# Kernel optimization log

Hardware: AMD Instinct MI355X
Metric: run time of the kernel (lower is better)

Reference implementation:

```python
import jax, jax.numpy as jnp
import numpy as np

B, C, H, W = 8, 512, 64, 64
RED = 4
CR = C // RED  # 128

def setup_inputs() -> dict:
    key = jax.random.key(0)
    k1, k2, k3 = jax.random.split(key, 3)
    x = jax.random.normal(k1, (B, C, H, W), dtype=jnp.float32)
    # conv_in: 1x1 conv, no bias -> weight [3*CR, C]
    w_in = jax.random.normal(k2, (3 * CR, C), dtype=jnp.float32) * 0.02
    # conv_out: 1x1 conv, no bias -> weight [C, CR]
    w_out = jax.random.normal(k3, (C, CR), dtype=jnp.float32) * 0.02
    return {"x": x, "w_in": w_in, "w_out": w_out}

def reference(x, w_in, w_out):
    b, c, h, w = x.shape
    n = h * w
    xf = x.reshape(b, c, n)                         # flatten spatial -> [B,C,N]
    proj = jnp.einsum('oc,bcn->bon', w_in, xf)      # 1x1 conv_in -> [B,3*CR,N]
    emb_a, emb_b, g = jnp.split(proj, 3, axis=1)    # each [B,CR,N]
    # unscaled full self-attention over N spatial tokens
    weights = jnp.einsum('bcn,bcm->bnm', emb_a, emb_b)   # [B,N,N]
    weights = jax.nn.softmax(weights, axis=2)
    y = jnp.einsum('bnm,bcm->bnc', weights, g)           # [B,N,CR]
    y = jnp.einsum('oc,bnc->bon', w_out, y)              # 1x1 conv_out -> [B,C,N]
    return x + y.reshape(b, c, h, w)
```

## Files before the change

### kernel.cpp

```cpp
#include <hip/hip_runtime.h>


typedef __attribute__((ext_vector_type(8))) short short8;
typedef __attribute__((ext_vector_type(4))) float f32x4;
typedef __attribute__((ext_vector_type(16))) float f32x16;
typedef __attribute__((ext_vector_type(2))) unsigned int uint2v;

__device__ inline unsigned bfr(float f) {
  union { float f; unsigned u; } v; v.f = f;
  return v.u + 0x8000u;
}
__device__ inline unsigned short f2bf(float f) { return (unsigned short)(bfr(f) >> 16); }
__device__ inline unsigned pack2(float a, float b) {
  return __builtin_amdgcn_perm(bfr(b), bfr(a), 0x07060302u);
}
__device__ inline unsigned cvtpk(float a, float b) {
  unsigned r;
  asm("v_cvt_pk_bf16_f32 %0, %1, %2" : "=v"(r) : "v"(a), "v"(b));
  return r;
}
__device__ inline int sw(int row, int col, int stride_halves) {
  return row * stride_halves + ((((col >> 3) ^ (row & 7)) << 3) | (col & 7));
}
__device__ inline void load_lds16(const void* g, void* l) {
  __builtin_amdgcn_global_load_lds(
      (const __attribute__((address_space(1))) unsigned int*)g,
      (__attribute__((address_space(3))) unsigned int*)l, 16, 0, 0);
}

__global__ __launch_bounds__(256) void k_prep(const float* __restrict__ w_in,
                                              const float* __restrict__ w_out,
                                              unsigned short* __restrict__ wi,
                                              unsigned short* __restrict__ wo) {
  int i = blockIdx.x * 256 + threadIdx.x;
  const float* src;
  unsigned short* dst;
  int base;
  float s = 1.0f;
  if (i < 24576) {
    src = w_in;  dst = wi; base = i * 8;
    if (base < 128 * 512) s = 1.4426950408889634f;
  } else {
    src = w_out; dst = wo; base = (i - 24576) * 8;
  }
  float4 d0 = *(const float4*)&src[base];
  float4 d1 = *(const float4*)&src[base + 4];
  d0.x *= s; d0.y *= s; d0.z *= s; d0.w *= s;
  d1.x *= s; d1.y *= s; d1.z *= s; d1.w *= s;
  uint4 p;
  p.x = pack2(d0.x, d0.y); p.y = pack2(d0.z, d0.w);
  p.z = pack2(d1.x, d1.y); p.w = pack2(d1.z, d1.w);
  *(uint4*)&dst[base] = p;
}

__global__ __launch_bounds__(256, 2) void k_proj(const float* __restrict__ x,
                                                 const unsigned short* __restrict__ wi,
                                                 unsigned short* __restrict__ aq,
                                                 unsigned short* __restrict__ Kf,
                                                 unsigned short* __restrict__ Vf) {
  __shared__ unsigned short A_lds[384 * 64];
  __shared__ unsigned short B_lds[64 * 64];
  const int t = threadIdx.x;
  const int lane = t & 63;
  const int w = t >> 6;
  const int l15 = lane & 15;
  const int quad = lane >> 4;
  const int tl = blockIdx.x;
  const int n0 = tl * 64;
  const int b = blockIdx.y;
  const int ch8g = t >> 5;
  const int tp = t & 31;

  f32x4 acc[6][4];
#pragma unroll
  for (int i = 0; i < 6; i++)
#pragma unroll
    for (int j = 0; j < 4; j++) acc[i][j] = (f32x4)0.f;

  float2 d[8];
#pragma unroll
  for (int j = 0; j < 8; j++)
    d[j] = *(const float2*)&x[((size_t)(b * 512 + ch8g * 8 + j)) * 4096 + n0 + tp * 2];

  for (int k0 = 0; k0 < 512; k0 += 64) {
#pragma unroll
    for (int j = 0; j < 12; j++) {
      int row = w * 96 + j * 8 + (lane >> 3);
      int gs = (lane & 7) ^ (row & 7);
      load_lds16(&wi[(size_t)row * 512 + k0 + gs * 8],
                 (void*)&A_lds[(w * 96 + j * 8) * 64]);
    }
#pragma unroll
    for (int i = 0; i < 2; i++) {
      int r = tp * 2 + i;
      uint4 pv;
      if (i == 0) {
        pv.x = pack2(d[0].x, d[1].x); pv.y = pack2(d[2].x, d[3].x);
        pv.z = pack2(d[4].x, d[5].x); pv.w = pack2(d[6].x, d[7].x);
      } else {
        pv.x = pack2(d[0].y, d[1].y); pv.y = pack2(d[2].y, d[3].y);
        pv.z = pack2(d[4].y, d[5].y); pv.w = pack2(d[6].y, d[7].y);
      }
      *(uint4*)&B_lds[sw(r, ch8g * 8, 64)] = pv;
    }
    if (k0 + 64 < 512) {
#pragma unroll
      for (int j = 0; j < 8; j++)
        d[j] = *(const float2*)&x[((size_t)(b * 512 + k0 + 64 + ch8g * 8 + j)) * 4096 + n0 + tp * 2];
    }
    __syncthreads();
#pragma unroll
    for (int kk = 0; kk < 64; kk += 32) {
      short8 a[6];
#pragma unroll
      for (int m = 0; m < 6; m++)
        a[m] = *(const short8*)&A_lds[sw(w * 96 + m * 16 + l15, kk + quad * 8, 64)];
#pragma unroll
      for (int ns = 0; ns < 4; ns++) {
        short8 bb = *(const short8*)&B_lds[sw(ns * 16 + l15, kk + quad * 8, 64)];
#pragma unroll
        for (int m = 0; m < 6; m++)
          acc[m][ns] = __builtin_amdgcn_mfma_f32_16x16x32_bf16(a[m], bb, acc[m][ns], 0, 0, 0);
      }
    }
    __syncthreads();
  }
  const size_t tbase = ((size_t)(b * 64 + tl)) * 8192;
#pragma unroll
  for (int m = 0; m < 6; m++) {
    int o = w * 96 + m * 16 + quad * 4;
    if (o < 128) {
#pragma unroll
      for (int ns = 0; ns < 4; ns++) {
        int n = n0 + ns * 16 + l15;
        uint2 p;
        p.x = pack2(acc[m][ns][0], acc[m][ns][1]);
        p.y = pack2(acc[m][ns][2], acc[m][ns][3]);
        *(uint2*)&aq[((size_t)(b * 4096 + n)) * 128 + o] = p;
      }
    } else if (o < 256) {
      int c = o - 128;
      int ksc = c >> 4, hk = (c >> 3) & 1, e0 = c & 7;
#pragma unroll
      for (int ns = 0; ns < 4; ns++) {
        int key = ns * 16 + l15;
        int ck = (key >> 5) * 8 + ksc;
        int lane_k = hk * 32 + (key & 31);
        uint2 p;
        p.x = pack2(acc[m][ns][0], acc[m][ns][1]);
        p.y = pack2(acc[m][ns][2], acc[m][ns][3]);
        *(uint2*)&Kf[tbase + ck * 512 + lane_k * 8 + e0] = p;
      }
    } else {
      int cb = o - 256;
#pragma unroll
      for (int ns = 0; ns < 4; ns++) {
        int key = ns * 16 + l15;
        int g8 = key >> 3;
        int e = key & 7;
        size_t kb = tbase + (size_t)((g8 & 1) * 32) * 8 + e + (size_t)(g8 >> 1) * 512;
#pragma unroll
        for (int r = 0; r < 4; r++) {
          int c = cb + r;
          Vf[kb + (size_t)(c >> 5) * 4 * 512 + (size_t)(c & 31) * 8] = f2bf(acc[m][ns][r]);
        }
      }
    }
  }
}

__global__ __launch_bounds__(512, 2) void k_attn(const unsigned short* __restrict__ aq,
                                                 const unsigned short* __restrict__ Kf,
                                                 const unsigned short* __restrict__ Vf,
                                                 unsigned short* __restrict__ yt) {
  __shared__ uint4 smem4[65536 / 16];
  unsigned short* smem_h = (unsigned short*)smem4;
  float* Obuf = (float*)smem4;
  float* lsumbuf = (float*)((char*)smem4 + 33024);
  unsigned* Pbuf = (unsigned*)((char*)smem4 + 33280);

  const int t = threadIdx.x;
  const int lane = t & 63;
  const int w = t >> 6;
  const int wr = w & 1;
  const int wc = w >> 1;
  const int l31 = lane & 31;
  const int h = lane >> 5;
  const int b = blockIdx.x & 7;
  const int q0 = (blockIdx.x >> 3) * 128;

  short8 qf[8];
  {
    const unsigned short* qp = &aq[((size_t)(b * 4096 + q0 + wc * 32 + l31)) * 128 + h * 8];
#pragma unroll
    for (int ks = 0; ks < 8; ks++) qf[ks] = *(const short8*)&qp[ks * 16];
  }

  auto dma_tile = [&](int tl, int buf) {
    unsigned short* Kb = smem_h + buf * 8192;
    unsigned short* Vb = smem_h + 16384 + buf * 8192;
    const unsigned short* Ks = &Kf[((size_t)(b * 64 + tl)) * 8192];
    const unsigned short* Vs = &Vf[((size_t)(b * 64 + tl)) * 8192];
#pragma unroll
    for (int j = 0; j < 2; j++) {
      int ck = w * 2 + j;
      load_lds16(&Ks[ck * 512 + lane * 8], (void*)&Kb[ck * 512]);
      load_lds16(&Vs[ck * 512 + lane * 8], (void*)&Vb[ck * 512]);
    }
  };

  f32x16 O[4];
#pragma unroll
  for (int i = 0; i < 4; i++) O[i] = (f32x16)0.f;
  float ls0 = 0.f, ls1 = 0.f, ls2 = 0.f, ls3 = 0.f;

  dma_tile(0, 0);
  __syncthreads();

  for (int it = 0; it < 64; ++it) {
    if (it < 63) dma_tile(it + 1, (it + 1) & 1);
    const unsigned short* Kc = smem_h + (it & 1) * 8192;
    const unsigned short* Vc = smem_h + 16384 + (it & 1) * 8192;

    f32x16 accS = (f32x16)0.f;
    __builtin_amdgcn_s_setprio(1);
#pragma unroll
    for (int ks = 0; ks < 8; ks++) {
      short8 ak = *(const short8*)&Kc[(wr * 8 + ks) * 512 + lane * 8];
      accS = __builtin_amdgcn_mfma_f32_32x32x16_bf16(ak, qf[ks], accS, 0, 0, 0);
    }
    __builtin_amdgcn_s_setprio(0);

    float ps[16];
#pragma unroll
    for (int r = 0; r < 16; r++) ps[r] = __builtin_amdgcn_exp2f(accS[r]);
    ls0 += ps[0] + ps[4];  ls1 += ps[1] + ps[5];
    ls2 += ps[2] + ps[6];  ls3 += ps[3] + ps[7];
    ls0 += ps[8] + ps[12]; ls1 += ps[9] + ps[13];
    ls2 += ps[10] + ps[14]; ls3 += ps[11] + ps[15];
    unsigned u[8];
#pragma unroll
    for (int i = 0; i < 8; i++) u[i] = cvtpk(ps[2 * i], ps[2 * i + 1]);

    short8 pfrag[2];
#pragma unroll
    for (int f = 0; f < 2; f++) {
      uint2v r02 = __builtin_amdgcn_permlane32_swap(u[4 * f + 0], u[4 * f + 2], false, false);
      uint2v r13 = __builtin_amdgcn_permlane32_swap(u[4 * f + 1], u[4 * f + 3], false, false);
      union { unsigned uu[4]; short8 s; } cv;
      cv.uu[0] = r02[0]; cv.uu[1] = r13[0]; cv.uu[2] = r02[1]; cv.uu[3] = r13[1];
      pfrag[f] = cv.s;
    }

    __builtin_amdgcn_s_setprio(1);
#pragma unroll
    for (int ct = 0; ct < 4; ct++) {
#pragma unroll
      for (int f = 0; f < 2; f++) {
        short8 av = *(const short8*)&Vc[(ct * 4 + wr * 2 + f) * 512 + lane * 8];
        O[ct] = __builtin_amdgcn_mfma_f32_32x32x16_bf16(av, pfrag[f], O[ct], 0, 0, 0);
      }
    }
    __builtin_amdgcn_s_setprio(0);
    __syncthreads();
  }

  float lsum = (ls0 + ls1) + (ls2 + ls3);
  lsum += __shfl_xor(lsum, 32);
#pragma unroll
  for (int p = 0; p < 2; ++p) {
    const bool act = (wc >> 1) == p;
    const int q = (wc & 1) * 32 + l31;
    if (act && wr == 0) {
#pragma unroll
      for (int ct = 0; ct < 4; ct++)
#pragma unroll
        for (int r = 0; r < 16; r++) {
          int c = ct * 32 + (r & 3) + 8 * (r >> 2) + 4 * h;
          Obuf[q * 129 + c] = O[ct][r];
        }
      if (h == 0) lsumbuf[q] = lsum;
    }
    __syncthreads();
    if (act && wr == 1) {
      float linv = 1.f / (lsum + lsumbuf[q]);
#pragma unroll
      for (int ct = 0; ct < 4; ct++)
#pragma unroll
        for (int r = 0; r < 16; r += 2) {
          int c = ct * 32 + (r & 3) + 8 * (r >> 2) + 4 * h;
          float v0 = (Obuf[q * 129 + c] + O[ct][r]) * linv;
          float v1 = (Obuf[q * 129 + c + 1] + O[ct][r + 1]) * linv;
          Pbuf[q * 65 + (c >> 1)] = pack2(v0, v1);
        }
    }
    __syncthreads();
    {
      int qq = t >> 3, seg = t & 7;
      unsigned* yrow = (unsigned*)&yt[((size_t)(b * 4096 + q0 + p * 64 + qq)) * 128];
#pragma unroll
      for (int i = 0; i < 2; i++) {
        int base = qq * 65 + seg * 8 + i * 4;
        uint4 v;
        v.x = Pbuf[base + 0];
        v.y = Pbuf[base + 1];
        v.z = Pbuf[base + 2];
        v.w = Pbuf[base + 3];
        *(uint4*)&yrow[seg * 8 + i * 4] = v;
      }
    }
  }
}

__global__ __launch_bounds__(256) void k_out(const float* __restrict__ x,
                                             const unsigned short* __restrict__ wo,
                                             const unsigned short* __restrict__ yt,
                                             float* __restrict__ out) {
  __shared__ unsigned short A_lds[128 * 128];
  __shared__ unsigned short B_lds[64 * 128];
  const int t = threadIdx.x;
  const int lane = t & 63;
  const int w = t >> 6;
  const int l15 = lane & 15;
  const int quad = lane >> 4;
  const int id = blockIdx.x;
  const int b = id & 7;
  const int rest = id >> 3;
  const int o0 = (rest & 3) * 128;
  const int n0 = (rest >> 2) * 64;

#pragma unroll
  for (int j = 0; j < 8; j++) {
    int row = w * 32 + j * 4 + (lane >> 4);
    int gs = (lane & 15) ^ (row & 7);
    load_lds16(&wo[(size_t)(o0 + row) * 128 + gs * 8],
               (void*)&A_lds[(w * 32 + j * 4) * 128]);
  }
#pragma unroll
  for (int j = 0; j < 4; j++) {
    int row = w * 16 + j * 4 + (lane >> 4);
    int gs = (lane & 15) ^ (row & 7);
    load_lds16(&yt[((size_t)(b * 4096 + n0 + row)) * 128 + gs * 8],
               (void*)&B_lds[(w * 16 + j * 4) * 128]);
  }
  __syncthreads();

  f32x4 acc[2][4];
#pragma unroll
  for (int i = 0; i < 2; i++)
#pragma unroll
    for (int j = 0; j < 4; j++) acc[i][j] = (f32x4)0.f;
#pragma unroll
  for (int ks = 0; ks < 4; ks++) {
    short8 a0 = *(const short8*)&A_lds[sw(w * 32 + l15, ks * 32 + quad * 8, 128)];
    short8 a1 = *(const short8*)&A_lds[sw(w * 32 + 16 + l15, ks * 32 + quad * 8, 128)];
#pragma unroll
    for (int ns = 0; ns < 4; ns++) {
      short8 bb = *(const short8*)&B_lds[sw(ns * 16 + l15, ks * 32 + quad * 8, 128)];
      acc[0][ns] = __builtin_amdgcn_mfma_f32_16x16x32_bf16(a0, bb, acc[0][ns], 0, 0, 0);
      acc[1][ns] = __builtin_amdgcn_mfma_f32_16x16x32_bf16(a1, bb, acc[1][ns], 0, 0, 0);
    }
  }
#pragma unroll
  for (int ms = 0; ms < 2; ms++) {
    int o = o0 + w * 32 + ms * 16 + quad * 4;
#pragma unroll
    for (int ns = 0; ns < 4; ns++) {
      int n = n0 + ns * 16 + l15;
#pragma unroll
      for (int r = 0; r < 4; r++) {
        size_t off = ((size_t)(b * 512 + o + r)) * 4096 + n;
        out[off] = x[off] + acc[ms][ns][r];
      }
    }
  }
}

extern "C" void kernel_launch(void* const* d_in, const int* in_sizes, int n_in,
                              void* d_out, int out_size, void* d_ws, size_t ws_size,
                              hipStream_t stream) {
  const float* x = (const float*)d_in[0];
  const float* w_in = (const float*)d_in[1];
  const float* w_out = (const float*)d_in[2];
  float* out = (float*)d_out;

  unsigned short* aq = (unsigned short*)d_ws;
  unsigned short* Kf = aq + (size_t)8 * 4096 * 128;
  unsigned short* Vf = Kf + (size_t)8 * 64 * 8192;
  unsigned short* yt = Vf + (size_t)8 * 64 * 8192;
  unsigned short* wi = yt + (size_t)8 * 4096 * 128;
  unsigned short* wo = wi + (size_t)384 * 512;

  k_prep<<<128, 256, 0, stream>>>(w_in, w_out, wi, wo);
  k_proj<<<dim3(64, 8), 256, 0, stream>>>(x, wi, aq, Kf, Vf);
  k_attn<<<dim3(256), 512, 0, stream>>>(aq, Kf, Vf, yt);
  k_out<<<2048, 256, 0, stream>>>(x, wo, yt, out);
}
```

Before: 215.4 us.

## Software-pipeline attention loop: overlap next QK^T with previous PV and softmax

Restructures the attention main loop so each iteration computes S for tile it while doing the P·V MFMAs for tile it-1 with the probabilities from the previous iteration. K and V loads are split so V for tile it is fetched one step behind K. The exp/convert/permlane softmax work can then interleave with independent MFMAs instead of sitting between dependent matrix phases. This adds a prologue and an epilogue, keeps an extra P fragment live (more register pressure), and changes the buffer timing.

Result: no change. 211.4 us (-1.9%).

```diff
diff --git a/kernel.cpp b/kernel.cpp
--- a/kernel.cpp
+++ b/kernel.cpp
@@ -196,16 +196,22 @@
     for (int ks = 0; ks < 8; ks++) qf[ks] = *(const short8*)&qp[ks * 16];
   }
 
-  auto dma_tile = [&](int tl, int buf) {
+  auto dma_k = [&](int tl, int buf) {
     unsigned short* Kb = smem_h + buf * 8192;
-    unsigned short* Vb = smem_h + 16384 + buf * 8192;
     const unsigned short* Ks = &Kf[((size_t)(b * 64 + tl)) * 8192];
-    const unsigned short* Vs = &Vf[((size_t)(b * 64 + tl)) * 8192];
 #pragma unroll
     for (int j = 0; j < 2; j++) {
       int ck = w * 2 + j;
       load_lds16(&Ks[ck * 512 + lane * 8], (void*)&Kb[ck * 512]);
-      load_lds16(&Vs[ck * 512 + lane * 8], (void*)&Vb[ck * 512]);
+    }
+  };
+  auto dma_v = [&](int tl, int buf) {
+    unsigned short* Vb = smem_h + 16384 + buf * 8192;
+    const unsigned short* Vs = &Vf[((size_t)(b * 64 + tl)) * 8192];
+#pragma unroll
+    for (int j = 0; j < 2; j++) {
+      int cv = w * 2 + j;
+      load_lds16(&Vs[cv * 512 + lane * 8], (void*)&Vb[cv * 512]);
     }
   };
 
@@ -213,24 +219,28 @@
 #pragma unroll
   for (int i = 0; i < 4; i++) O[i] = (f32x16)0.f;
   float ls0 = 0.f, ls1 = 0.f, ls2 = 0.f, ls3 = 0.f;
-
-  dma_tile(0, 0);
-  __syncthreads();
-
-  for (int it = 0; it < 64; ++it) {
-    if (it < 63) dma_tile(it + 1, (it + 1) & 1);
-    const unsigned short* Kc = smem_h + (it & 1) * 8192;
-    const unsigned short* Vc = smem_h + 16384 + (it & 1) * 8192;
-
+  short8 pfP[2];
+
+  auto computeS = [&](const unsigned short* Kc) -> f32x16 {
     f32x16 accS = (f32x16)0.f;
-    __builtin_amdgcn_s_setprio(1);
 #pragma unroll
     for (int ks = 0; ks < 8; ks++) {
       short8 ak = *(const short8*)&Kc[(wr * 8 + ks) * 512 + lane * 8];
       accS = __builtin_amdgcn_mfma_f32_32x32x16_bf16(ak, qf[ks], accS, 0, 0, 0);
     }
-    __builtin_amdgcn_s_setprio(0);
-
+    return accS;
+  };
+  auto computePV = [&](const unsigned short* Vc, const short8 pf[2]) {
+#pragma unroll
+    for (int ct = 0; ct < 4; ct++) {
+#pragma unroll
+      for (int f = 0; f < 2; f++) {
+        short8 av = *(const short8*)&Vc[(ct * 4 + wr * 2 + f) * 512 + lane * 8];
+        O[ct] = __builtin_amdgcn_mfma_f32_32x32x16_bf16(av, pf[f], O[ct], 0, 0, 0);
+      }
+    }
+  };
+  auto softmax = [&](const f32x16& accS, short8 pf[2]) {
     float ps[16];
 #pragma unroll
     for (int r = 0; r < 16; r++) ps[r] = __builtin_amdgcn_exp2f(accS[r]);
@@ -241,29 +251,48 @@
     unsigned u[8];
 #pragma unroll
     for (int i = 0; i < 8; i++) u[i] = cvtpk(ps[2 * i], ps[2 * i + 1]);
-
-    short8 pfrag[2];
 #pragma unroll
     for (int f = 0; f < 2; f++) {
       uint2v r02 = __builtin_amdgcn_permlane32_swap(u[4 * f + 0], u[4 * f + 2], false, false);
       uint2v r13 = __builtin_amdgcn_permlane32_swap(u[4 * f + 1], u[4 * f + 3], false, false);
       union { unsigned uu[4]; short8 s; } cv;
       cv.uu[0] = r02[0]; cv.uu[1] = r13[0]; cv.uu[2] = r02[1]; cv.uu[3] = r13[1];
-      pfrag[f] = cv.s;
-    }
-
+      pf[f] = cv.s;
+    }
+  };
+
+  dma_k(0, 0);
+  dma_v(0, 0);
+  __syncthreads();
+
+  {
+    dma_k(1, 1);
     __builtin_amdgcn_s_setprio(1);
-#pragma unroll
-    for (int ct = 0; ct < 4; ct++) {
-#pragma unroll
-      for (int f = 0; f < 2; f++) {
-        short8 av = *(const short8*)&Vc[(ct * 4 + wr * 2 + f) * 512 + lane * 8];
-        O[ct] = __builtin_amdgcn_mfma_f32_32x32x16_bf16(av, pfrag[f], O[ct], 0, 0, 0);
-      }
-    }
+    f32x16 accS = computeS(smem_h);
     __builtin_amdgcn_s_setprio(0);
-    __syncthreads();
-  }
+    softmax(accS, pfP);
+    __syncthreads();
+  }
+
+  for (int it = 1; it < 64; ++it) {
+    if (it < 63) dma_k(it + 1, (it + 1) & 1);
+    dma_v(it, it & 1);
+    const unsigned short* Kc = smem_h + (it & 1) * 8192;
+    const unsigned short* Vp = smem_h + 16384 + ((it - 1) & 1) * 8192;
+    __builtin_amdgcn_s_setprio(1);
+    f32x16 accS = computeS(Kc);
+    computePV(Vp, pfP);
+    __builtin_amdgcn_s_setprio(0);
+    softmax(accS, pfP);
+    __syncthreads();
+  }
+
+  {
+    __builtin_amdgcn_s_setprio(1);
+    computePV(smem_h + 16384 + 8192, pfP);
+    __builtin_amdgcn_s_setprio(0);
+  }
+  __syncthreads();
 
   float lsum = (ls0 + ls1) + (ls2 + ls3);
   lsum += __shfl_xor(lsum, 32);
```
